# Kernel optimization log

Hardware: AMD Instinct MI355X
Metric: run time of the kernel (lower is better)

## Reference

```python
import jax, jax.numpy as jnp
import numpy as np

B, S, H = 2, 2048, 4096
NH, NKV, D = 32, 8, 128  # heads, kv heads, head_dim


def rotate_half(x):
    x1, x2 = jnp.split(x, 2, axis=-1)
    return jnp.concatenate((-x2, x1), axis=-1)


def setup_inputs() -> dict:
    key = jax.random.key(0)
    ks = jax.random.split(key, 5)
    hidden_states = jax.random.normal(ks[0], (B, S, H), jnp.float32) * 0.02
    wq = jax.random.normal(ks[1], (H, NH * D), jnp.float32) * 0.02
    wk = jax.random.normal(ks[2], (H, NKV * D), jnp.float32) * 0.02
    wv = jax.random.normal(ks[3], (H, NKV * D), jnp.float32) * 0.02
    wo = jax.random.normal(ks[4], (NH * D, H), jnp.float32) * 0.02
    # Llama rotary cache: emb = cat(freqs, freqs); cos/sin shape [S, D]
    inv_freq = 1.0 / (10000.0 ** (jnp.arange(0, D, 2, dtype=jnp.float32) / D))
    t = jnp.arange(S, dtype=jnp.float32)
    freqs = jnp.einsum('i,j->ij', t, inv_freq)
    emb = jnp.concatenate((freqs, freqs), axis=-1)
    cos, sin = jnp.cos(emb), jnp.sin(emb)
    # additive causal mask [S, S]
    causal = jnp.tril(jnp.ones((S, S), dtype=bool))
    attn_mask = jnp.where(causal, 0.0, -1e9).astype(jnp.float32)
    return {'hidden_states': hidden_states, 'wq': wq, 'wk': wk, 'wv': wv,
            'wo': wo, 'cos': cos, 'sin': sin, 'attn_mask': attn_mask}


def reference(hidden_states, wq, wk, wv, wo, cos, sin, attn_mask):
    b, s, _ = hidden_states.shape
    q = (hidden_states @ wq).reshape(b, s, NH, D)   # [b,s,nh,d]
    k = (hidden_states @ wk).reshape(b, s, NKV, D)  # [b,s,nkv,d]
    v = (hidden_states @ wv).reshape(b, s, NKV, D)
    c = cos[None, :, None, :]  # [1,s,1,d]
    sn = sin[None, :, None, :]
    q = q * c + rotate_half(q) * sn
    k = k * c + rotate_half(k) * sn
    # GQA: repeat KV heads to match query heads
    grp = NH // NKV
    k = jnp.repeat(k, grp, axis=2)
    v = jnp.repeat(v, grp, axis=2)
    scale = 1.0 / np.sqrt(D).astype(np.float32)
    scores = jnp.einsum('bqhd,bkhd->bhqk', q, k) * scale
    scores = scores + attn_mask[None, None, :, :]
    probs = jax.nn.softmax(scores, axis=-1)
    out = jnp.einsum('bhqk,bkhd->bqhd', probs, v).reshape(b, s, NH * D)
    return out @ wo
```

## Files before the change

### kernel.cpp

```cpp
#include <hip/hip_runtime.h>

typedef __attribute__((ext_vector_type(8))) short short8;
typedef __attribute__((ext_vector_type(4))) float f32x4;
typedef __attribute__((ext_vector_type(4))) int int4v;

__device__ __forceinline__ float bf2f(unsigned short u) {
  unsigned int x = ((unsigned int)u) << 16;
  float f;
  __builtin_memcpy(&f, &x, 4);
  return f;
}
__device__ __forceinline__ unsigned short f2bf(float f) {
  unsigned int x;
  __builtin_memcpy(&x, &f, 4);
  unsigned int r = (x + 0x7FFFu + ((x >> 16) & 1u)) >> 16;
  return (unsigned short)r;
}
__device__ __forceinline__ unsigned int cvtpk_bf16(float lo, float hi) {
  unsigned int r;
  asm("v_cvt_pk_bf16_f32 %0, %1, %2" : "=v"(r) : "v"(lo), "v"(hi));
  return r;
}
__device__ __forceinline__ float exp2_hw(float x) {
  float r;
  asm("v_exp_f32 %0, %1" : "=v"(r) : "v"(x));
  return r;
}
__device__ __forceinline__ int4v s8_to_i4(short8 v) {
  int4v r;
  __builtin_memcpy(&r, &v, 16);
  return r;
}
__device__ __forceinline__ short8 i4_to_s8(int4v v) {
  short8 r;
  __builtin_memcpy(&r, &v, 16);
  return r;
}
__device__ __forceinline__ short8 ld8_f32(const float* p) {
  f32x4 x = *(const f32x4*)p;
  f32x4 y = *(const f32x4*)(p + 4);
  short8 r;
  r[0] = (short)f2bf(x[0]); r[1] = (short)f2bf(x[1]);
  r[2] = (short)f2bf(x[2]); r[3] = (short)f2bf(x[3]);
  r[4] = (short)f2bf(y[0]); r[5] = (short)f2bf(y[1]);
  r[6] = (short)f2bf(y[2]); r[7] = (short)f2bf(y[3]);
  return r;
}

__device__ __forceinline__ void async16(unsigned short* lds, const unsigned short* g) {
  __builtin_amdgcn_global_load_lds(
      (const __attribute__((address_space(1))) void*)g,
      (__attribute__((address_space(3))) void*)lds, 16, 0, 0);
}

__global__ void downcast_f2b(const float* __restrict__ in,
                             unsigned short* __restrict__ out, int n8) {
  int i = blockIdx.x * 256 + threadIdx.x;
  if (i >= n8) return;
  *(short8*)(out + (size_t)i * 8) = ld8_f32(in + (size_t)i * 8);
}

__global__ void transpose_f2b(const float* __restrict__ in,
                              unsigned short* __restrict__ out, int R, int Ccols) {
  __shared__ unsigned short tile[32][33];
  const int c0 = blockIdx.x * 32;
  const int r0 = blockIdx.y * 32;
  const int tx = threadIdx.x, ty = threadIdx.y;
#pragma unroll
  for (int i = 0; i < 32; i += 8)
    tile[ty + i][tx] = f2bf(in[(size_t)(r0 + ty + i) * Ccols + (c0 + tx)]);
  __syncthreads();
#pragma unroll
  for (int i = 0; i < 32; i += 8)
    out[(size_t)(c0 + ty + i) * R + (r0 + tx)] = tile[tx][ty + i];
}

#define MFMA16(AF, B0, B1, N0, N1)                                                   \
  _Pragma("unroll") for (int mi = 0; mi < 8; mi++) {                                 \
    acc[mi][N0] = __builtin_amdgcn_mfma_f32_16x16x32_bf16(AF[mi], B0, acc[mi][N0], 0, 0, 0); \
    acc[mi][N1] = __builtin_amdgcn_mfma_f32_16x16x32_bf16(AF[mi], B1, acc[mi][N1], 0, 0, 0); \
  }

#define STAGE8(BUF, SLOT, BASE, KOFF)                                     \
  do {                                                                    \
    async16(&lds[BUF][SLOT][tid * 8], (BASE) + (KOFF));                   \
    async16(&lds[BUF][SLOT][4096 + tid * 8], (BASE) + Kstep128 + (KOFF)); \
  } while (0)

#define BAR8 asm volatile("s_barrier" ::: "memory")

#define TILE8(CUR, UU, S0, S123, VM)                                                   \
  do {                                                                                 \
    const int kb = (UU)*64;                                                            \
    short8 af[8], b0, b1;                                                              \
                                                                       \
    _Pragma("unroll") for (int mi = 0; mi < 8; mi++)                                   \
        af[mi] = *(const short8*)(&lds[CUR][0][(wr * 128 + mi * 16 + fr) * 32 + fragoff]); \
    b0 = *(const short8*)(&lds[CUR][2][(wc * 64 + 0 * 16 + fr) * 32 + fragoff]);       \
    b1 = *(const short8*)(&lds[CUR][2][(wc * 64 + 1 * 16 + fr) * 32 + fragoff]);       \
    if (S0) STAGE8((CUR) ^ 1, 3, Bbase, kb + 96);                                      \
    BAR8;                                                                              \
    __builtin_amdgcn_s_setprio(1);                                                     \
    MFMA16(af, b0, b1, 0, 1);                                                          \
    __builtin_amdgcn_s_setprio(0);                                                     \
    BAR8;                                                                              \
                                                                       \
    b0 = *(const short8*)(&lds[CUR][2][(wc * 64 + 2 * 16 + fr) * 32 + fragoff]);       \
    b1 = *(const short8*)(&lds[CUR][2][(wc * 64 + 3 * 16 + fr) * 32 + fragoff]);       \
    if (S123) STAGE8(CUR, 0, Abase, kb + 128);                                         \
    BAR8;                                                                              \
    __builtin_amdgcn_s_setprio(1);                                                     \
    MFMA16(af, b0, b1, 2, 3);                                                          \
    __builtin_amdgcn_s_setprio(0);                                                     \
    BAR8;                                                                              \
                                                                       \
    _Pragma("unroll") for (int mi = 0; mi < 8; mi++)                                   \
        af[mi] = *(const short8*)(&lds[CUR][1][(wr * 128 + mi * 16 + fr) * 32 + fragoff]); \
    b0 = *(const short8*)(&lds[CUR][3][(wc * 64 + 0 * 16 + fr) * 32 + fragoff]);       \
    b1 = *(const short8*)(&lds[CUR][3][(wc * 64 + 1 * 16 + fr) * 32 + fragoff]);       \
    if (S123) STAGE8(CUR, 2, Bbase, kb + 128);                                         \
    BAR8;                                                                              \
    __builtin_amdgcn_s_setprio(1);                                                     \
    MFMA16(af, b0, b1, 0, 1);                                                          \
    __builtin_amdgcn_s_setprio(0);                                                     \
    BAR8;                                                                              \
                                                                       \
    b0 = *(const short8*)(&lds[CUR][3][(wc * 64 + 2 * 16 + fr) * 32 + fragoff]);       \
    b1 = *(const short8*)(&lds[CUR][3][(wc * 64 + 3 * 16 + fr) * 32 + fragoff]);       \
    if (S123) STAGE8(CUR, 1, Abase, kb + 160);                                         \
    BAR8;                                                                              \
    __builtin_amdgcn_s_setprio(1);                                                     \
    MFMA16(af, b0, b1, 2, 3);                                                          \
    __builtin_amdgcn_s_setprio(0);                                                     \
    if ((VM) == 6) {                                                                   \
      asm volatile("s_waitcnt vmcnt(6)" ::: "memory");                                 \
      __builtin_amdgcn_sched_barrier(0);                                               \
    } else if ((VM) == 0) {                                                            \
      asm volatile("s_waitcnt vmcnt(0)" ::: "memory");                                 \
      __builtin_amdgcn_sched_barrier(0);                                               \
    }                                                                                  \
    BAR8;                                                                              \
  } while (0)

template <int CF32>
__global__ __launch_bounds__(512, 2) void gemm8p(
    const unsigned short* __restrict__ A, const unsigned short* __restrict__ BT,
    void* __restrict__ Cp, int M, int N, int K) {
  alignas(16) __shared__ unsigned short lds[2][4][8192];
  const int tid = threadIdx.x;
  const int l = tid & 63;
  const int wv = tid >> 6;
  const int wr = wv >> 2, wc = wv & 3;

  const int nwg = gridDim.x * gridDim.y;
  int id = blockIdx.y * gridDim.x + blockIdx.x;
  id = (id & 7) * (nwg >> 3) + (id >> 3);
  const int bm = (id % gridDim.x) * 256;
  const int bn = (id / gridDim.x) * 256;

  const int fr = l & 15, hi = l >> 4;
  const int fragoff = ((hi ^ (((fr >> 3) & 1) << 1)) << 3);
  const int srow = tid >> 2;
  const int scol = (((tid & 3) ^ (((tid >> 5) & 1) << 1)) << 3);
  const unsigned short* Abase = A + (size_t)(bm + srow) * K + scol;
  const unsigned short* Bbase = BT + (size_t)(bn + srow) * K + scol;
  const size_t Kstep128 = (size_t)128 * K;

  f32x4 acc[8][4] = {};
  const int nt = K >> 6;

  STAGE8(0, 0, Abase, 0);
  STAGE8(0, 2, Bbase, 0);
  STAGE8(0, 1, Abase, 32);
  STAGE8(0, 3, Bbase, 32);
  STAGE8(1, 0, Abase, 64);
  STAGE8(1, 2, Bbase, 64);
  STAGE8(1, 1, Abase, 96);
  asm volatile("s_waitcnt vmcnt(6)" ::: "memory");
  __builtin_amdgcn_sched_barrier(0);
  BAR8;

  int U = 0;
  for (; U + 3 < nt; U += 2) {
    TILE8(0, U, 1, 1, 6);
    TILE8(1, U + 1, 1, 1, 6);
  }
  TILE8(0, nt - 2, 1, 0, 0);
  TILE8(1, nt - 1, 0, 0, -1);

  const int er = hi << 2;
#pragma unroll
  for (int mi = 0; mi < 8; mi++) {
#pragma unroll
    for (int ni = 0; ni < 4; ni++) {
      int row = bm + wr * 128 + mi * 16 + er;
      int col = bn + wc * 64 + ni * 16 + fr;
#pragma unroll
      for (int r = 0; r < 4; r++) {
        if constexpr (CF32)
          ((float*)Cp)[(size_t)(row + r) * N + col] = acc[mi][ni][r];
        else
          ((unsigned short*)Cp)[(size_t)(row + r) * N + col] = f2bf(acc[mi][ni][r]);
      }
    }
  }
}

__global__ void rope_kernel(unsigned short* __restrict__ buf,
                            const float* __restrict__ cosb,
                            const float* __restrict__ sinb,
                            int nh_shift, int rstride, int total, float oscale) {
  int gid = blockIdx.x * 256 + threadIdx.x;
  if (gid >= total) return;
  int dblk = gid & 7;
  int u = gid >> 3;
  int head = u & ((1 << nh_shift) - 1);
  int token = u >> nh_shift;
  int s = token & 2047;
  int d0 = dblk << 3;
  unsigned short* p0 = buf + (size_t)token * rstride + (head << 7) + d0;
  unsigned short* p1 = p0 + 64;
  const float* cp = cosb + s * 128 + d0;
  const float* sp = sinb + s * 128 + d0;
  short8 a = *(const short8*)p0;
  short8 bq = *(const short8*)p1;
  f32x4 c0 = *(const f32x4*)cp, c1 = *(const f32x4*)(cp + 4);
  f32x4 s0 = *(const f32x4*)sp, s1 = *(const f32x4*)(sp + 4);
  short8 o0, o1;
#pragma unroll
  for (int j = 0; j < 8; j++) {
    float x0 = bf2f((unsigned short)a[j]);
    float x1 = bf2f((unsigned short)bq[j]);
    float c = (j < 4) ? c0[j & 3] : c1[j & 3];
    float sn = (j < 4) ? s0[j & 3] : s1[j & 3];
    o0[j] = (short)f2bf((x0 * c - x1 * sn) * oscale);
    o1[j] = (short)f2bf((x1 * c + x0 * sn) * oscale);
  }
  *(short8*)p0 = o0;
  *(short8*)p1 = o1;
}

#define NEGBIG -30000.0f

__device__ __forceinline__ int vswz(int d) { return (((d >> 3) ^ d) & 7) << 2; }

__global__ __launch_bounds__(256, 2) void flash_attn(
    const unsigned short* __restrict__ Q, const unsigned short* __restrict__ KV,
    unsigned short* __restrict__ O) {
  alignas(16) __shared__ unsigned short lK[64 * 128];
  alignas(16) __shared__ unsigned int lV[128 * 32];

  const int tid = threadIdx.x;
  const int lane = tid & 63;
  const int w = tid >> 6;
  const int b = blockIdx.z;
  const int h = blockIdx.y;
  const int xa = blockIdx.x;
  const int kvh = h >> 2;

  const int fr = lane & 15;
  const int hi = lane >> 4;
  const int fk8 = hi << 3;
  const int hi4 = hi << 2;

  const int srow = tid >> 4;
  const int sc8 = (tid & 15) << 3;
  const int parity = srow & 1;

  const unsigned short* Kbp = KV + (size_t)(b * 2048) * 2048 + kvh * 128;
  const unsigned short* Vbp = Kbp + 1024;

  for (int pass = 0; pass < 2; pass++) {
    const int x = pass ? (15 - xa) : xa;
    const int q0 = x * 128;
    const int nt = 2 * x + 2;

    short8 qf[2][4];
#pragma unroll
    for (int qsub = 0; qsub < 2; qsub++) {
      const unsigned short* qb =
          Q + (size_t)(b * 2048 + q0 + w * 32 + qsub * 16 + fr) * 4096 + h * 128 + fk8;
#pragma unroll
      for (int ks = 0; ks < 4; ks++) qf[qsub][ks] = *(const short8*)(qb + ks * 32);
    }

    f32x4 oacc[2][8] = {};
    float m2[2] = {NEGBIG, NEGBIG};
    float ls[2] = {0.f, 0.f};

    short8 kreg[4], vreg[4];
#pragma unroll
    for (int rep = 0; rep < 4; rep++) {
      kreg[rep] = *(const short8*)(Kbp + (size_t)(rep * 16 + srow) * 2048 + sc8);
      vreg[rep] = *(const short8*)(Vbp + (size_t)(rep * 16 + srow) * 2048 + sc8);
    }

    for (int t = 0; t < nt; t++) {
      __syncthreads();
#pragma unroll
      for (int rep = 0; rep < 4; rep++)
        *(short8*)(lK + (rep * 16 + srow) * 128 + (sc8 ^ ((srow & 7) << 3))) = kreg[rep];
#pragma unroll
      for (int rep = 0; rep < 4; rep++) {
        int4v own = s8_to_i4(vreg[rep]);
        int4v oth;
#pragma unroll
        for (int q = 0; q < 4; q++) oth[q] = __shfl_xor(own[q], 16);
        unsigned int oA = parity ? (unsigned)own[2] : (unsigned)own[0];
        unsigned int oB = parity ? (unsigned)own[3] : (unsigned)own[1];
        unsigned int tA = parity ? (unsigned)oth[2] : (unsigned)oth[0];
        unsigned int tB = parity ? (unsigned)oth[3] : (unsigned)oth[1];
        unsigned int evA = parity ? tA : oA, odA = parity ? oA : tA;
        unsigned int evB = parity ? tB : oB, odB = parity ? oB : tB;
        int d0 = sc8 + (parity << 2);
        int kvp = rep * 8 + (srow >> 1);
        lV[(d0 + 0) * 32 + (kvp ^ vswz(d0 + 0))] = (evA & 0xFFFFu) | (odA << 16);
        lV[(d0 + 1) * 32 + (kvp ^ vswz(d0 + 1))] = (evA >> 16) | (odA & 0xFFFF0000u);
        lV[(d0 + 2) * 32 + (kvp ^ vswz(d0 + 2))] = (evB & 0xFFFFu) | (odB << 16);
        lV[(d0 + 3) * 32 + (kvp ^ vswz(d0 + 3))] = (evB >> 16) | (odB & 0xFFFF0000u);
      }
      __syncthreads();

      if (t + 1 < nt) {
        const int kv1 = (t + 1) * 64;
#pragma unroll
        for (int rep = 0; rep < 4; rep++) {
          kreg[rep] = *(const short8*)(Kbp + (size_t)(kv1 + rep * 16 + srow) * 2048 + sc8);
          vreg[rep] = *(const short8*)(Vbp + (size_t)(kv1 + rep * 16 + srow) * 2048 + sc8);
        }
      } else if (pass == 0) {
#pragma unroll
        for (int rep = 0; rep < 4; rep++) {
          kreg[rep] = *(const short8*)(Kbp + (size_t)(rep * 16 + srow) * 2048 + sc8);
          vreg[rep] = *(const short8*)(Vbp + (size_t)(rep * 16 + srow) * 2048 + sc8);
        }
      }

      f32x4 sacc[2][4] = {};
      __builtin_amdgcn_s_setprio(1);
#pragma unroll
      for (int fc = 0; fc < 4; fc++)
#pragma unroll
        for (int ks = 0; ks < 4; ks++) {
          short8 bk = *(const short8*)(lK + (fc * 16 + fr) * 128 +
                                       ((ks * 32 + fk8) ^ ((fr & 7) << 3)));
          sacc[0][fc] = __builtin_amdgcn_mfma_f32_16x16x32_bf16(bk, qf[0][ks], sacc[0][fc], 0, 0, 0);
          sacc[1][fc] = __builtin_amdgcn_mfma_f32_16x16x32_bf16(bk, qf[1][ks], sacc[1][fc], 0, 0, 0);
        }
      __builtin_amdgcn_s_setprio(0);

      const bool diag = (t >= nt - 2);
      const int kvb = t * 64;
      unsigned int pk[2][4][2];

#pragma unroll
      for (int qsub = 0; qsub < 2; qsub++) {
        const int q = q0 + w * 32 + qsub * 16 + fr;
        float sv[4][4];
#pragma unroll
        for (int fc = 0; fc < 4; fc++)
#pragma unroll
          for (int r = 0; r < 4; r++) {
            float xx = sacc[qsub][fc][r];
            if (diag && (kvb + fc * 16 + hi4 + r > q)) xx = NEGBIG;
            sv[fc][r] = xx;
          }
        float mx = sv[0][0];
#pragma unroll
        for (int fc = 0; fc < 4; fc++)
#pragma unroll
          for (int r = 0; r < 4; r++) mx = fmaxf(mx, sv[fc][r]);
        mx = fmaxf(mx, __shfl_xor(mx, 16));
        mx = fmaxf(mx, __shfl_xor(mx, 32));
        if (__any(mx > m2[qsub] + 8.0f)) {
          float mnew = fmaxf(m2[qsub], mx);
          float alpha = exp2_hw(m2[qsub] - mnew);
          m2[qsub] = mnew;
          ls[qsub] *= alpha;
          f32x4 av;
#pragma unroll
          for (int r = 0; r < 4; r++) av[r] = __shfl(alpha, hi4 + r);
#pragma unroll
          for (int nf = 0; nf < 8; nf++) oacc[qsub][nf] *= av;
        }
        float rs = 0.f;
        float p[4][4];
#pragma unroll
        for (int fc = 0; fc < 4; fc++)
#pragma unroll
          for (int r = 0; r < 4; r++) {
            p[fc][r] = exp2_hw(sv[fc][r] - m2[qsub]);
            rs += p[fc][r];
          }
        rs += __shfl_xor(rs, 16);
        rs += __shfl_xor(rs, 32);
        ls[qsub] += rs;
#pragma unroll
        for (int fc = 0; fc < 4; fc++) {
          pk[qsub][fc][0] = cvtpk_bf16(p[fc][0], p[fc][1]);
          pk[qsub][fc][1] = cvtpk_bf16(p[fc][2], p[fc][3]);
        }
      }

      const int src0 = fr + ((hi & 1) << 5);
      const int src1 = src0 + 16;
#pragma unroll
      for (int kvs = 0; kvs < 2; kvs++) {
        unsigned int aw[2][4];
#pragma unroll
        for (int qsub = 0; qsub < 2; qsub++) {
#pragma unroll
          for (int jj = 0; jj < 4; jj++) {
            int src = (jj < 2) ? src0 : src1;
            int rr = jj & 1;
            unsigned int y0 = (unsigned)__shfl((int)pk[qsub][kvs * 2][rr], src);
            unsigned int y1 = (unsigned)__shfl((int)pk[qsub][kvs * 2 + 1][rr], src);
            aw[qsub][jj] = (hi >> 1) ? y1 : y0;
          }
        }
        int4v a0i = {(int)aw[0][0], (int)aw[0][1], (int)aw[0][2], (int)aw[0][3]};
        int4v a1i = {(int)aw[1][0], (int)aw[1][1], (int)aw[1][2], (int)aw[1][3]};
        short8 af0 = i4_to_s8(a0i), af1 = i4_to_s8(a1i);
        __builtin_amdgcn_s_setprio(1);
#pragma unroll
        for (int nf = 0; nf < 8; nf++) {
          int row = nf * 16 + fr;
          int4v bvw = *(const int4v*)(lV + row * 32 + ((kvs * 16 + hi4) ^ vswz(row)));
          short8 bv = i4_to_s8(bvw);
          oacc[0][nf] = __builtin_amdgcn_mfma_f32_16x16x32_bf16(af0, bv, oacc[0][nf], 0, 0, 0);
          oacc[1][nf] = __builtin_amdgcn_mfma_f32_16x16x32_bf16(af1, bv, oacc[1][nf], 0, 0, 0);
        }
        __builtin_amdgcn_s_setprio(0);
      }
    }

#pragma unroll
    for (int qsub = 0; qsub < 2; qsub++) {
      f32x4 iv;
#pragma unroll
      for (int r = 0; r < 4; r++) iv[r] = 1.0f / __shfl(ls[qsub], hi4 + r);
#pragma unroll
      for (int r = 0; r < 4; r++) {
        unsigned short* op =
            O + (size_t)(b * 2048 + q0 + w * 32 + qsub * 16 + hi4 + r) * 4096 + h * 128 + fr;
#pragma unroll
        for (int nf = 0; nf < 8; nf++) op[nf * 16] = f2bf(oacc[qsub][nf][r] * iv[r]);
      }
    }
  }
}

extern "C" void kernel_launch(void* const* d_in, const int* in_sizes, int n_in,
                              void* d_out, int out_size, void* d_ws, size_t ws_size,
                              hipStream_t stream) {
  const float* hs = (const float*)d_in[0];
  const float* wq = (const float*)d_in[1];
  const float* wk = (const float*)d_in[2];
  const float* wv = (const float*)d_in[3];
  const float* wo = (const float*)d_in[4];
  const float* cosb = (const float*)d_in[5];
  const float* sinb = (const float*)d_in[6];

  unsigned short* ws = (unsigned short*)d_ws;
  unsigned short* T1 = ws;
  unsigned short* T2 = T1 + 16777216;
  unsigned short* T3 = T2 + 4194304;
  unsigned short* Qb = T3 + 4194304;
  unsigned short* KVb = Qb + 16777216;
  unsigned short* Ob = KVb + 8388608;

  unsigned short* hsb = (unsigned short*)d_out;

  dim3 tb(32, 8);
  downcast_f2b<<<8192, 256, 0, stream>>>(hs, hsb, 2097152);
  transpose_f2b<<<dim3(128, 128), tb, 0, stream>>>(wq, T1, 4096, 4096);
  transpose_f2b<<<dim3(32, 128), tb, 0, stream>>>(wk, T2, 4096, 1024);
  transpose_f2b<<<dim3(32, 128), tb, 0, stream>>>(wv, T3, 4096, 1024);

  gemm8p<0><<<dim3(16, 16), 512, 0, stream>>>(hsb, T1, Qb, 4096, 4096, 4096);
  gemm8p<0><<<dim3(16, 8), 512, 0, stream>>>(hsb, T2, KVb, 4096, 2048, 4096);

  transpose_f2b<<<dim3(128, 128), tb, 0, stream>>>(wo, T1, 4096, 4096);

  const float qscale = 0.08838834764831845f * 1.4426950408889634f;
  rope_kernel<<<4096, 256, 0, stream>>>(Qb, cosb, sinb, 5, 4096, 4096 * 32 * 8, qscale);
  rope_kernel<<<1024, 256, 0, stream>>>(KVb, cosb, sinb, 3, 2048, 4096 * 8 * 8, 1.0f);

  flash_attn<<<dim3(8, 32, 2), 256, 0, stream>>>(Qb, KVb, Ob);

  gemm8p<1><<<dim3(16, 16), 512, 0, stream>>>(Ob, T1, (float*)d_out, 4096, 4096, 4096);
}
```

Measured before the change: 540.7 us.

## Fuse Q and KV projections into one GEMM, merge RoPE kernels, widen transpose

The Q and K/V projection GEMMs become a single 6144-wide GEMM writing into one interleaved QKV buffer. This relies on T1, T2 and T3 being contiguous, so the transposed wq/wk/wv form one weight matrix. The two RoPE launches are merged into one kernel that branches on the global index, and flash attention now reads Q, K and V with a 6144 row stride. The weight transpose moves to 64x64 tiles with float4 loads and 16-byte bf16 stores. Together these cut launch count, fill the GPU better in one larger GEMM, and make the transposes more bandwidth-efficient, at the cost of wider strides in attention loads.

```diff
diff --git a/kernel.cpp b/kernel.cpp
--- a/kernel.cpp
+++ b/kernel.cpp
@@ -60,19 +60,30 @@
   *(short8*)(out + (size_t)i * 8) = ld8_f32(in + (size_t)i * 8);
 }
 
-__global__ void transpose_f2b(const float* __restrict__ in,
-                              unsigned short* __restrict__ out, int R, int Ccols) {
-  __shared__ unsigned short tile[32][33];
-  const int c0 = blockIdx.x * 32;
-  const int r0 = blockIdx.y * 32;
-  const int tx = threadIdx.x, ty = threadIdx.y;
-#pragma unroll
-  for (int i = 0; i < 32; i += 8)
-    tile[ty + i][tx] = f2bf(in[(size_t)(r0 + ty + i) * Ccols + (c0 + tx)]);
+__global__ void transpose64_f2b(const float* __restrict__ in,
+                                unsigned short* __restrict__ out, int R, int C) {
+  alignas(16) __shared__ unsigned short t[64][72];
+  const int c0 = blockIdx.x * 64;
+  const int r0 = blockIdx.y * 64;
+  const int tid = threadIdx.x;
+  const int rr = tid >> 4;
+  const int cc = (tid & 15) << 2;
+#pragma unroll
+  for (int i = 0; i < 4; i++) {
+    int r = rr + i * 16;
+    f32x4 v = *(const f32x4*)(in + (size_t)(r0 + r) * C + c0 + cc);
+#pragma unroll
+    for (int j = 0; j < 4; j++) t[cc + j][r] = f2bf(v[j]);
+  }
   __syncthreads();
-#pragma unroll
-  for (int i = 0; i < 32; i += 8)
-    out[(size_t)(c0 + ty + i) * R + (r0 + tx)] = tile[tx][ty + i];
+  const int seg = tid & 7;
+  const int cr = tid >> 3;
+#pragma unroll
+  for (int i = 0; i < 2; i++) {
+    int c = cr + i * 32;
+    short8 w = *(const short8*)&t[c][seg * 8];
+    *(short8*)(out + (size_t)(c0 + c) * R + r0 + seg * 8) = w;
+  }
 }
 
 #define MFMA16(AF, B0, B1, N0, N1)                                                   \
@@ -206,19 +217,22 @@
   }
 }
 
-__global__ void rope_kernel(unsigned short* __restrict__ buf,
-                            const float* __restrict__ cosb,
-                            const float* __restrict__ sinb,
-                            int nh_shift, int rstride, int total, float oscale) {
+__global__ void rope_qk(unsigned short* __restrict__ qkv,
+                        const float* __restrict__ cosb,
+                        const float* __restrict__ sinb, float qscale) {
   int gid = blockIdx.x * 256 + threadIdx.x;
-  if (gid >= total) return;
-  int dblk = gid & 7;
-  int u = gid >> 3;
-  int head = u & ((1 << nh_shift) - 1);
-  int token = u >> nh_shift;
+  const int isK = gid >= 1048576;
+  int g = isK ? gid - 1048576 : gid;
+  const int nhs = isK ? 3 : 5;
+  const int base = isK ? 4096 : 0;
+  const float sc = isK ? 1.0f : qscale;
+  int dblk = g & 7;
+  int u2 = g >> 3;
+  int head = u2 & ((1 << nhs) - 1);
+  int token = u2 >> nhs;
   int s = token & 2047;
   int d0 = dblk << 3;
-  unsigned short* p0 = buf + (size_t)token * rstride + (head << 7) + d0;
+  unsigned short* p0 = qkv + (size_t)token * 6144 + base + (head << 7) + d0;
   unsigned short* p1 = p0 + 64;
   const float* cp = cosb + s * 128 + d0;
   const float* sp = sinb + s * 128 + d0;
@@ -233,8 +247,8 @@
     float x1 = bf2f((unsigned short)bq[j]);
     float c = (j < 4) ? c0[j & 3] : c1[j & 3];
     float sn = (j < 4) ? s0[j & 3] : s1[j & 3];
-    o0[j] = (short)f2bf((x0 * c - x1 * sn) * oscale);
-    o1[j] = (short)f2bf((x1 * c + x0 * sn) * oscale);
+    o0[j] = (short)f2bf((x0 * c - x1 * sn) * sc);
+    o1[j] = (short)f2bf((x1 * c + x0 * sn) * sc);
   }
   *(short8*)p0 = o0;
   *(short8*)p1 = o1;
@@ -245,8 +259,7 @@
 __device__ __forceinline__ int vswz(int d) { return (((d >> 3) ^ d) & 7) << 2; }
 
 __global__ __launch_bounds__(256, 2) void flash_attn(
-    const unsigned short* __restrict__ Q, const unsigned short* __restrict__ KV,
-    unsigned short* __restrict__ O) {
+    const unsigned short* __restrict__ QKV, unsigned short* __restrict__ O) {
   alignas(16) __shared__ unsigned short lK[64 * 128];
   alignas(16) __shared__ unsigned int lV[128 * 32];
 
@@ -267,7 +280,7 @@
   const int sc8 = (tid & 15) << 3;
   const int parity = srow & 1;
 
-  const unsigned short* Kbp = KV + (size_t)(b * 2048) * 2048 + kvh * 128;
+  const unsigned short* Kbp = QKV + (size_t)(b * 2048) * 6144 + 4096 + kvh * 128;
   const unsigned short* Vbp = Kbp + 1024;
 
   for (int pass = 0; pass < 2; pass++) {
@@ -279,7 +292,7 @@
 #pragma unroll
     for (int qsub = 0; qsub < 2; qsub++) {
       const unsigned short* qb =
-          Q + (size_t)(b * 2048 + q0 + w * 32 + qsub * 16 + fr) * 4096 + h * 128 + fk8;
+          QKV + (size_t)(b * 2048 + q0 + w * 32 + qsub * 16 + fr) * 6144 + h * 128 + fk8;
 #pragma unroll
       for (int ks = 0; ks < 4; ks++) qf[qsub][ks] = *(const short8*)(qb + ks * 32);
     }
@@ -291,8 +304,8 @@
     short8 kreg[4], vreg[4];
 #pragma unroll
     for (int rep = 0; rep < 4; rep++) {
-      kreg[rep] = *(const short8*)(Kbp + (size_t)(rep * 16 + srow) * 2048 + sc8);
-      vreg[rep] = *(const short8*)(Vbp + (size_t)(rep * 16 + srow) * 2048 + sc8);
+      kreg[rep] = *(const short8*)(Kbp + (size_t)(rep * 16 + srow) * 6144 + sc8);
+      vreg[rep] = *(const short8*)(Vbp + (size_t)(rep * 16 + srow) * 6144 + sc8);
     }
 
     for (int t = 0; t < nt; t++) {
@@ -325,14 +338,14 @@
         const int kv1 = (t + 1) * 64;
 #pragma unroll
         for (int rep = 0; rep < 4; rep++) {
-          kreg[rep] = *(const short8*)(Kbp + (size_t)(kv1 + rep * 16 + srow) * 2048 + sc8);
-          vreg[rep] = *(const short8*)(Vbp + (size_t)(kv1 + rep * 16 + srow) * 2048 + sc8);
+          kreg[rep] = *(const short8*)(Kbp + (size_t)(kv1 + rep * 16 + srow) * 6144 + sc8);
+          vreg[rep] = *(const short8*)(Vbp + (size_t)(kv1 + rep * 16 + srow) * 6144 + sc8);
         }
       } else if (pass == 0) {
 #pragma unroll
         for (int rep = 0; rep < 4; rep++) {
-          kreg[rep] = *(const short8*)(Kbp + (size_t)(rep * 16 + srow) * 2048 + sc8);
-          vreg[rep] = *(const short8*)(Vbp + (size_t)(rep * 16 + srow) * 2048 + sc8);
+          kreg[rep] = *(const short8*)(Kbp + (size_t)(rep * 16 + srow) * 6144 + sc8);
+          vreg[rep] = *(const short8*)(Vbp + (size_t)(rep * 16 + srow) * 6144 + sc8);
         }
       }
 
@@ -465,28 +478,24 @@
   unsigned short* T1 = ws;
   unsigned short* T2 = T1 + 16777216;
   unsigned short* T3 = T2 + 4194304;
-  unsigned short* Qb = T3 + 4194304;
-  unsigned short* KVb = Qb + 16777216;
-  unsigned short* Ob = KVb + 8388608;
+  unsigned short* QKV = T3 + 4194304;
+  unsigned short* Ob = QKV + 25165824;
 
   unsigned short* hsb = (unsigned short*)d_out;
 
-  dim3 tb(32, 8);
   downcast_f2b<<<8192, 256, 0, stream>>>(hs, hsb, 2097152);
-  transpose_f2b<<<dim3(128, 128), tb, 0, stream>>>(wq, T1, 4096, 4096);
-  transpose_f2b<<<dim3(32, 128), tb, 0, stream>>>(wk, T2, 4096, 1024);
-  transpose_f2b<<<dim3(32, 128), tb, 0, stream>>>(wv, T3, 4096, 1024);
-
-  gemm8p<0><<<dim3(16, 16), 512, 0, stream>>>(hsb, T1, Qb, 4096, 4096, 4096);
-  gemm8p<0><<<dim3(16, 8), 512, 0, stream>>>(hsb, T2, KVb, 4096, 2048, 4096);
-
-  transpose_f2b<<<dim3(128, 128), tb, 0, stream>>>(wo, T1, 4096, 4096);
+  transpose64_f2b<<<dim3(64, 64), 256, 0, stream>>>(wq, T1, 4096, 4096);
+  transpose64_f2b<<<dim3(16, 64), 256, 0, stream>>>(wk, T2, 4096, 1024);
+  transpose64_f2b<<<dim3(16, 64), 256, 0, stream>>>(wv, T3, 4096, 1024);
+
+  gemm8p<0><<<dim3(16, 24), 512, 0, stream>>>(hsb, T1, QKV, 4096, 6144, 4096);
+
+  transpose64_f2b<<<dim3(64, 64), 256, 0, stream>>>(wo, T1, 4096, 4096);
 
   const float qscale = 0.08838834764831845f * 1.4426950408889634f;
-  rope_kernel<<<4096, 256, 0, stream>>>(Qb, cosb, sinb, 5, 4096, 4096 * 32 * 8, qscale);
-  rope_kernel<<<1024, 256, 0, stream>>>(KVb, cosb, sinb, 3, 2048, 4096 * 8 * 8, 1.0f);
-
-  flash_attn<<<dim3(8, 32, 2), 256, 0, stream>>>(Qb, KVb, Ob);
+  rope_qk<<<5120, 256, 0, stream>>>(QKV, cosb, sinb, qscale);
+
+  flash_attn<<<dim3(8, 32, 2), 256, 0, stream>>>(QKV, Ob);
 
   gemm8p<1><<<dim3(16, 16), 512, 0, stream>>>(Ob, T1, (float*)d_out, 4096, 4096, 4096);
 }
```

After: 529.3 us. -2.1%, faster.
